# Kernel tuning notes

Measured on AMD Instinct MI355X. Metric: run time of the kernel, lower is better.

Reference implementation:

```python
import jax, jax.numpy as jnp
import numpy as np

N = 50000        # nodes
E = 1600000      # edges (avg degree 32)
H = 128          # hidden_channels == num_filters
G = 50           # num_gaussians
L = 5            # num_interactions
CUTOFF = 4.5
VOCAB = 100
LOG2 = float(np.log(2.0))


def setup_inputs() -> dict:
    key = jax.random.key(0)
    ks = jax.random.split(key, 12)
    s = 1.0 / np.sqrt(H)
    sg = 1.0 / np.sqrt(G)
    atomic_numbers = jax.random.randint(ks[0], (N,), 0, VOCAB, dtype=jnp.int32)
    edge_index = jax.random.randint(ks[1], (2, E), 0, N, dtype=jnp.int32)
    edge_attr = jax.random.uniform(ks[2], (E,), dtype=jnp.float32)
    emb = jax.random.normal(ks[3], (VOCAB, H), dtype=jnp.float32) * 0.1
    emb = emb.at[0].set(0.0)  # padding_idx=0
    Wi = jax.random.normal(ks[4], (L, H, H), dtype=jnp.float32) * s
    bi = jnp.zeros((L, H), dtype=jnp.float32)
    Wn = jax.random.normal(ks[5], (L, G, H), dtype=jnp.float32) * sg
    bn = jnp.zeros((L, H), dtype=jnp.float32)
    Wo = jax.random.normal(ks[6], (L, H, H), dtype=jnp.float32) * s
    bo = jnp.zeros((L, H), dtype=jnp.float32)
    Wl = jax.random.normal(ks[7], (L, H, H), dtype=jnp.float32) * s
    bl = jnp.zeros((L, H), dtype=jnp.float32)
    return {"atomic_numbers": atomic_numbers, "edge_index": edge_index,
            "edge_attr": edge_attr, "emb": emb,
            "Wi": Wi, "bi": bi, "Wn": Wn, "bn": bn,
            "Wo": Wo, "bo": bo, "Wl": Wl, "bl": bl}


def _gaussian_smearing(dist):
    offsets = jnp.linspace(0.0, CUTOFF, G, dtype=jnp.float32)
    coeff = -0.5 / (offsets[1] - offsets[0]) ** 2
    return jnp.exp(coeff * (dist[:, None] - offsets[None, :]) ** 2)  # [E, G]


def reference(atomic_numbers, edge_index, edge_attr, emb,
              Wi, bi, Wn, bn, Wo, bo, Wl, bl):
    src, dst = edge_index[0], edge_index[1]
    x = emb[atomic_numbers]                      # [N, H]
    gauss = _gaussian_smearing(edge_attr)        # [E, G]
    C = 0.5 * (jnp.cos(edge_attr * jnp.pi / CUTOFF) + 1.0)  # cosine cutoff [E]
    for l in range(L):
        W = (gauss @ Wn[l] + bn[l]) * C[:, None]   # edge filters [E, H]
        h = x @ Wi[l] + bi[l]                       # [N, H]
        msg = h[src] * W                            # gather + filter [E, H]
        agg = jax.ops.segment_sum(msg, dst, num_segments=N)  # scatter-add [N, H]
        h = agg @ Wo[l] + bo[l]
        h = jax.nn.softplus(h) - LOG2               # shifted softplus
        h = h @ Wl[l] + bl[l]
        x = x + h                                   # residual
    return x
```

## Files before the change

### kernel.cpp

```cpp
#include <hip/hip_runtime.h>
#include <hip/hip_bf16.h>

#define HDIM 128
#define NG 50
#define NL 5
#define TBN 4096
#define CAP 96
#define CAPB 9000
#define CHUNK 8192

static constexpr float CUTOFF_F = 4.5f;
static constexpr float PI_F = 3.14159265358979323846f;
static constexpr float LN2_F = 0.6931471805599453f;

typedef __attribute__((ext_vector_type(8))) short bf16x8;
typedef __attribute__((ext_vector_type(4))) float f32x4;

__device__ __forceinline__ unsigned f2bfbits(float f) {
    unsigned b = __float_as_uint(f);
    return (b + 0x7FFFu + ((b >> 16) & 1u)) >> 16;
}
__device__ __forceinline__ float bflo(unsigned u) { return __uint_as_float(u << 16); }
__device__ __forceinline__ float bfhi(unsigned u) { return __uint_as_float(u & 0xFFFF0000u); }

__device__ __forceinline__ float softplus_shifted(float v) {
    return fmaxf(v, 0.0f) + log1pf(__expf(-fabsf(v))) - LN2_F;
}

__device__ __forceinline__ bf16x8 ldB(const unsigned short* __restrict__ W,
                                      int nn, int kc, int l4) {
    return *reinterpret_cast<const bf16x8*>(W + nn * HDIM + kc * 32 + l4 * 8);
}

__global__ __launch_bounds__(256) void embed_kernel(
    const int* __restrict__ an, const float* __restrict__ emb,
    float* __restrict__ x, int n)
{
    int idx = blockIdx.x * 256 + threadIdx.x;
    int total = n * (HDIM / 4);
    if (idx >= total) return;
    int i = idx >> 5;
    int j = idx & 31;
    int a = an[i];
    reinterpret_cast<float4*>(x)[(size_t)i * 32 + j] =
        reinterpret_cast<const float4*>(emb)[(size_t)a * 32 + j];
}

__global__ __launch_bounds__(256) void prep_weights(
    const float* __restrict__ Wi, const float* __restrict__ Wo,
    const float* __restrict__ Wl, unsigned short* __restrict__ Wt)
{
    int b = blockIdx.x;
    int l = b / 3, m = b % 3;
    const float* src = (m == 0 ? Wi : (m == 1 ? Wo : Wl)) + (size_t)l * HDIM * HDIM;
    unsigned short* dst = Wt + (size_t)b * HDIM * HDIM;
    for (int idx = threadIdx.x; idx < HDIM * HDIM; idx += 256) {
        int k = idx >> 7, n = idx & 127;
        dst[n * HDIM + k] = (unsigned short)f2bfbits(src[k * HDIM + n]);
    }
}

__global__ __launch_bounds__(128) void build_tables_all(
    const float* __restrict__ Wn, const float* __restrict__ bn,
    unsigned short* __restrict__ T)
{
    __shared__ float gs[NG];
    int p = blockIdx.x;
    int l = blockIdx.y;
    int j = threadIdx.x;
    const float* Wnl = Wn + (size_t)l * NG * HDIM;
    float d = (float)p * (1.0f / (float)TBN);
    if (j < NG) {
        const float delta = CUTOFF_F / (float)(NG - 1);
        const float coeff = -0.5f / (delta * delta);
        float t = d - (float)j * delta;
        gs[j] = expf(coeff * t * t);
    }
    __syncthreads();
    float acc = bn[(size_t)l * HDIM + j];
    #pragma unroll 10
    for (int g = 0; g < NG; ++g) acc = fmaf(gs[g], Wnl[g * HDIM + j], acc);
    acc *= 0.5f * (cosf(d * (PI_F / CUTOFF_F)) + 1.0f);
    T[((size_t)l * (TBN + 1) + p) * HDIM + j] = (unsigned short)f2bfbits(acc);
}

__global__ __launch_bounds__(512) void bucket_pass(
    const int* __restrict__ src, const int* __restrict__ dstp,
    const float* __restrict__ attr, int* __restrict__ gbase,
    uint2* __restrict__ buf, int E, int nbuck)
{
    __shared__ int hist[256], cur[256], base_l[256];
    const int tid = threadIdx.x;
    if (tid < 256) { hist[tid] = 0; cur[tid] = 0; }
    __syncthreads();
    const int e0 = blockIdx.x * CHUNK;
    const int e1 = min(e0 + CHUNK, E);
    for (int e = e0 + tid; e < e1; e += 512)
        atomicAdd(&hist[dstp[e] >> 8], 1);
    __syncthreads();
    if (tid < nbuck)
        base_l[tid] = hist[tid] ? atomicAdd(&gbase[tid], hist[tid]) : 0;
    __syncthreads();
    for (int e = e0 + tid; e < e1; e += 512) {
        int d = dstp[e];
        int b = d >> 8;
        int rank = atomicAdd(&cur[b], 1);
        int pos = base_l[b] + rank;
        unsigned ii = (unsigned)(int)fminf(attr[e] * (float)TBN + 0.5f, (float)TBN);
        if (pos < CAPB)
            buf[(size_t)b * CAPB + pos] = make_uint2((ii << 16) | (unsigned)src[e], (unsigned)d);
    }
}

__global__ __launch_bounds__(512) void bin_pass(
    const int* __restrict__ gtot, const uint2* __restrict__ buf,
    unsigned* __restrict__ sp, int* __restrict__ cnt, int N)
{
    __shared__ int cl[256];
    const int b = blockIdx.x;
    const int tid = threadIdx.x;
    if (tid < 256) cl[tid] = 0;
    __syncthreads();
    int total = gtot[b];
    if (total > CAPB) total = CAPB;
    const uint2* rb = buf + (size_t)b * CAPB;
    for (int i = tid; i < total; i += 512) {
        uint2 r = rb[i];
        int node = (int)r.y;
        int slot = atomicAdd(&cl[node & 255], 1);
        if (slot < CAP) sp[(size_t)node * CAP + slot] = r.x;
    }
    __syncthreads();
    if (tid < 256) {
        int node = b * 256 + tid;
        if (node < N) cnt[node] = min(cl[tid], CAP);
    }
}

__global__ __launch_bounds__(256) void mfma_gemm0(
    const float* __restrict__ A, const unsigned short* __restrict__ Wt,
    const float* __restrict__ bias, unsigned short* __restrict__ outp, int M)
{
    __shared__ unsigned short Al[64 * HDIM];
    __shared__ unsigned short Hs[64 * HDIM];
    const int tid = threadIdx.x;
    const int row0 = blockIdx.x * 64;

    #pragma unroll
    for (int it = 0; it < 8; ++it) {
        int idx = it * 256 + tid;
        int r = idx >> 5;
        int k2 = (idx & 31) * 8;
        int row = row0 + r;
        float4 v = make_float4(0.f, 0.f, 0.f, 0.f);
        if (row < M) v = reinterpret_cast<const float4*>(A)[(size_t)row * 32 + (idx & 31)];
        uint2 u;
        u.x = f2bfbits(v.x) | (f2bfbits(v.y) << 16);
        u.y = f2bfbits(v.z) | (f2bfbits(v.w) << 16);
        *reinterpret_cast<uint2*>(reinterpret_cast<char*>(Al) +
            r * 256 + (k2 ^ ((r & 7) << 4))) = u;
    }
    __syncthreads();

    const int wid = tid >> 6, lane = tid & 63;
    const int wr = wid >> 1, wc = wid & 1;
    const int l15 = lane & 15, l4 = lane >> 4;

    f32x4 acc[2][4] = {};
    bf16x8 afrag[2][4];
    #pragma unroll
    for (int m = 0; m < 2; ++m)
        #pragma unroll
        for (int kc = 0; kc < 4; ++kc) {
            int r = wr * 32 + m * 16 + l15;
            int k2 = (kc * 32 + l4 * 8) * 2;
            afrag[m][kc] = *reinterpret_cast<const bf16x8*>(
                reinterpret_cast<const char*>(Al) + r * 256 + (k2 ^ ((r & 7) << 4)));
        }
    #pragma unroll
    for (int n = 0; n < 4; ++n)
        #pragma unroll
        for (int kc = 0; kc < 4; ++kc) {
            bf16x8 bfrag = ldB(Wt, wc * 64 + n * 16 + l15, kc, l4);
            #pragma unroll
            for (int m = 0; m < 2; ++m)
                acc[m][n] = __builtin_amdgcn_mfma_f32_16x16x32_bf16(
                    afrag[m][kc], bfrag, acc[m][n], 0, 0, 0);
        }
    #pragma unroll
    for (int n = 0; n < 4; ++n) {
        int col = wc * 64 + n * 16 + l15;
        float bv = bias[col];
        #pragma unroll
        for (int m = 0; m < 2; ++m)
            #pragma unroll
            for (int r = 0; r < 4; ++r) {
                int rl = wr * 32 + m * 16 + l4 * 4 + r;
                Hs[rl * HDIM + col] = (unsigned short)f2bfbits(acc[m][n][r] + bv);
            }
    }
    __syncthreads();
    #pragma unroll
    for (int it = 0; it < 4; ++it) {
        int e = it * 256 + tid;
        int row = row0 + (e >> 4);
        if (row < M)
            reinterpret_cast<uint4*>(outp)[(size_t)row0 * 16 + e] =
                reinterpret_cast<const uint4*>(Hs)[e];
    }
}

template<int LAST>
__global__ __launch_bounds__(256) void gemm_fused(
    const unsigned short* __restrict__ aggb, const unsigned short* __restrict__ Wot,
    const float* __restrict__ bo, const unsigned short* __restrict__ Wlt,
    const float* __restrict__ bl, float* __restrict__ x,
    const unsigned short* __restrict__ Wit, const float* __restrict__ bi_,
    unsigned short* __restrict__ hb, int M)
{
    __shared__ unsigned short Al[64 * HDIM];
    __shared__ unsigned short Hs[64 * HDIM];
    const int tid = threadIdx.x;
    const int row0 = blockIdx.x * 64;

    #pragma unroll
    for (int it = 0; it < 4; ++it) {
        int idx = it * 256 + tid;
        int r = idx >> 4;
        int k2 = (idx & 15) * 16;
        int row = row0 + r;
        uint4 v = make_uint4(0, 0, 0, 0);
        if (row < M) v = reinterpret_cast<const uint4*>(aggb)[(size_t)row * 16 + (idx & 15)];
        *reinterpret_cast<uint4*>(reinterpret_cast<char*>(Al) +
            r * 256 + (k2 ^ ((r & 7) << 4))) = v;
    }
    __syncthreads();

    const int wid = tid >> 6, lane = tid & 63;
    const int wr = wid >> 1, wc = wid & 1;
    const int l15 = lane & 15, l4 = lane >> 4;

    f32x4 acc1[2][4] = {};
    bf16x8 afrag[2][4];
    #pragma unroll
    for (int m = 0; m < 2; ++m)
        #pragma unroll
        for (int kc = 0; kc < 4; ++kc) {
            int r = wr * 32 + m * 16 + l15;
            int k2 = (kc * 32 + l4 * 8) * 2;
            afrag[m][kc] = *reinterpret_cast<const bf16x8*>(
                reinterpret_cast<const char*>(Al) + r * 256 + (k2 ^ ((r & 7) << 4)));
        }
    #pragma unroll
    for (int n = 0; n < 4; ++n)
        #pragma unroll
        for (int kc = 0; kc < 4; ++kc) {
            bf16x8 bfrag = ldB(Wot, wc * 64 + n * 16 + l15, kc, l4);
            #pragma unroll
            for (int m = 0; m < 2; ++m)
                acc1[m][n] = __builtin_amdgcn_mfma_f32_16x16x32_bf16(
                    afrag[m][kc], bfrag, acc1[m][n], 0, 0, 0);
        }
    __syncthreads();

    #pragma unroll
    for (int n = 0; n < 4; ++n) {
        int col = wc * 64 + n * 16 + l15;
        float bv = bo[col];
        #pragma unroll
        for (int m = 0; m < 2; ++m)
            #pragma unroll
            for (int r = 0; r < 4; ++r) {
                int rl = wr * 32 + m * 16 + l4 * 4 + r;
                float v = softplus_shifted(acc1[m][n][r] + bv);
                *reinterpret_cast<unsigned short*>(reinterpret_cast<char*>(Al) +
                    rl * 256 + ((2 * col) ^ ((rl & 7) << 4))) = (unsigned short)f2bfbits(v);
            }
    }
    __syncthreads();

    f32x4 acc2[2][4] = {};
    #pragma unroll
    for (int m = 0; m < 2; ++m)
        #pragma unroll
        for (int kc = 0; kc < 4; ++kc) {
            int r = wr * 32 + m * 16 + l15;
            int k2 = (kc * 32 + l4 * 8) * 2;
            afrag[m][kc] = *reinterpret_cast<const bf16x8*>(
                reinterpret_cast<const char*>(Al) + r * 256 + (k2 ^ ((r & 7) << 4)));
        }
    #pragma unroll
    for (int n = 0; n < 4; ++n)
        #pragma unroll
        for (int kc = 0; kc < 4; ++kc) {
            bf16x8 bfrag = ldB(Wlt, wc * 64 + n * 16 + l15, kc, l4);
            #pragma unroll
            for (int m = 0; m < 2; ++m)
                acc2[m][n] = __builtin_amdgcn_mfma_f32_16x16x32_bf16(
                    afrag[m][kc], bfrag, acc2[m][n], 0, 0, 0);
        }
    __syncthreads();

    #pragma unroll
    for (int n = 0; n < 4; ++n) {
        int col = wc * 64 + n * 16 + l15;
        float bv = bl[col];
        #pragma unroll
        for (int m = 0; m < 2; ++m)
            #pragma unroll
            for (int r = 0; r < 4; ++r) {
                int rl = wr * 32 + m * 16 + l4 * 4 + r;
                int row = row0 + rl;
                float v = acc2[m][n][r] + bv;
                if (row < M) {
                    float* o = x + (size_t)row * HDIM + col;
                    v += *o;
                    *o = v;
                }
                if (!LAST)
                    *reinterpret_cast<unsigned short*>(reinterpret_cast<char*>(Al) +
                        rl * 256 + ((2 * col) ^ ((rl & 7) << 4))) = (unsigned short)f2bfbits(v);
            }
    }
    if (LAST) return;
    __syncthreads();

    f32x4 acc3[2][4] = {};
    #pragma unroll
    for (int m = 0; m < 2; ++m)
        #pragma unroll
        for (int kc = 0; kc < 4; ++kc) {
            int r = wr * 32 + m * 16 + l15;
            int k2 = (kc * 32 + l4 * 8) * 2;
            afrag[m][kc] = *reinterpret_cast<const bf16x8*>(
                reinterpret_cast<const char*>(Al) + r * 256 + (k2 ^ ((r & 7) << 4)));
        }
    #pragma unroll
    for (int n = 0; n < 4; ++n)
        #pragma unroll
        for (int kc = 0; kc < 4; ++kc) {
            bf16x8 bfrag = ldB(Wit, wc * 64 + n * 16 + l15, kc, l4);
            #pragma unroll
            for (int m = 0; m < 2; ++m)
                acc3[m][n] = __builtin_amdgcn_mfma_f32_16x16x32_bf16(
                    afrag[m][kc], bfrag, acc3[m][n], 0, 0, 0);
        }
    #pragma unroll
    for (int n = 0; n < 4; ++n) {
        int col = wc * 64 + n * 16 + l15;
        float bv = bi_[col];
        #pragma unroll
        for (int m = 0; m < 2; ++m)
            #pragma unroll
            for (int r = 0; r < 4; ++r) {
                int rl = wr * 32 + m * 16 + l4 * 4 + r;
                Hs[rl * HDIM + col] = (unsigned short)f2bfbits(acc3[m][n][r] + bv);
            }
    }
    __syncthreads();
    #pragma unroll
    for (int it = 0; it < 4; ++it) {
        int e = it * 256 + tid;
        int row = row0 + (e >> 4);
        if (row < M)
            reinterpret_cast<uint4*>(hb)[(size_t)row0 * 16 + e] =
                reinterpret_cast<const uint4*>(Hs)[e];
    }
}

__global__ __launch_bounds__(256) void agg_kernel(
    const int* __restrict__ cnt, const unsigned* __restrict__ sp,
    const unsigned short* __restrict__ T,
    const unsigned* __restrict__ hb,
    unsigned* __restrict__ aggb, int n)
{
    __shared__ float2 part[2][64];
    const int tid = threadIdx.x;
    const int lane = tid & 63;
    const int wv = tid >> 6;
    const int pair = wv >> 1, half = wv & 1;
    const int node = blockIdx.x * 2 + pair;

    int deg = (node < n) ? cnt[node] : 0;
    const unsigned* recs = sp + (size_t)node * CAP;
    int d2 = deg >> 1;
    int i  = half ? d2 : 0;
    int i1 = half ? deg : d2;
    float ax = 0.0f, ay = 0.0f;

    for (; i + 8 <= i1; i += 8) {
        unsigned rec[8], tv[8], hv[8];
        #pragma unroll
        for (int k = 0; k < 8; ++k) rec[k] = recs[i + k];
        #pragma unroll
        for (int k = 0; k < 8; ++k) {
            tv[k] = reinterpret_cast<const unsigned*>(T + (size_t)(rec[k] >> 16) * HDIM)[lane];
            hv[k] = hb[(size_t)(rec[k] & 0xFFFFu) * 64 + lane];
        }
        #pragma unroll
        for (int k = 0; k < 8; ++k) {
            ax = fmaf(bflo(hv[k]), bflo(tv[k]), ax);
            ay = fmaf(bfhi(hv[k]), bfhi(tv[k]), ay);
        }
    }
    if (i + 4 <= i1) {
        unsigned rec[4], tv[4], hv[4];
        #pragma unroll
        for (int k = 0; k < 4; ++k) rec[k] = recs[i + k];
        #pragma unroll
        for (int k = 0; k < 4; ++k) {
            tv[k] = reinterpret_cast<const unsigned*>(T + (size_t)(rec[k] >> 16) * HDIM)[lane];
            hv[k] = hb[(size_t)(rec[k] & 0xFFFFu) * 64 + lane];
        }
        #pragma unroll
        for (int k = 0; k < 4; ++k) {
            ax = fmaf(bflo(hv[k]), bflo(tv[k]), ax);
            ay = fmaf(bfhi(hv[k]), bfhi(tv[k]), ay);
        }
        i += 4;
    }
    for (; i < i1; ++i) {
        unsigned rec = recs[i];
        unsigned tvv = reinterpret_cast<const unsigned*>(T + (size_t)(rec >> 16) * HDIM)[lane];
        unsigned hvv = hb[(size_t)(rec & 0xFFFFu) * 64 + lane];
        ax = fmaf(bflo(hvv), bflo(tvv), ax);
        ay = fmaf(bfhi(hvv), bfhi(tvv), ay);
    }

    if (half) part[pair][lane] = make_float2(ax, ay);
    __syncthreads();
    if (!half && node < n) {
        float2 p = part[pair][lane];
        ax += p.x; ay += p.y;
        aggb[(size_t)node * 64 + lane] = f2bfbits(ax) | (f2bfbits(ay) << 16);
    }
}

extern "C" void kernel_launch(void* const* d_in, const int* in_sizes, int n_in,
                              void* d_out, int out_size, void* d_ws, size_t ws_size,
                              hipStream_t stream)
{
    const int*   an   = (const int*)d_in[0];
    const int*   ei   = (const int*)d_in[1];
    const float* attr = (const float*)d_in[2];
    const float* emb  = (const float*)d_in[3];
    const float* Wi   = (const float*)d_in[4];
    const float* bi   = (const float*)d_in[5];
    const float* Wn   = (const float*)d_in[6];
    const float* bn   = (const float*)d_in[7];
    const float* Wo   = (const float*)d_in[8];
    const float* bo   = (const float*)d_in[9];
    const float* Wl   = (const float*)d_in[10];
    const float* bl   = (const float*)d_in[11];

    const int N = in_sizes[0];
    const int E = in_sizes[2];
    const int* srcp = ei;
    const int* dstp = ei + E;
    const int nbuck = (N + 255) >> 8;

    float* x = (float*)d_out;

    char* w = (char*)d_ws;
    unsigned*       aggb = (unsigned*)w;      w += (size_t)N * HDIM * 2;
    unsigned*       hb   = (unsigned*)w;      w += (size_t)N * HDIM * 2;
    unsigned short* T    = (unsigned short*)w; w += (size_t)NL * (TBN + 1) * HDIM * 2;
    unsigned short* Wt   = (unsigned short*)w; w += (size_t)NL * 3 * HDIM * HDIM * 2;
    int*            cnt  = (int*)w;           w += (size_t)N * 4;
    int*            gbase= (int*)w;           w += 256 * 4;
    unsigned*       sp   = (unsigned*)w;      w += (size_t)N * CAP * 4;
    uint2*          buf  = (uint2*)aggb;

    prep_weights<<<NL * 3, 256, 0, stream>>>(Wi, Wo, Wl, Wt);
    embed_kernel<<<(N * 32 + 255) / 256, 256, 0, stream>>>(an, emb, x, N);
    build_tables_all<<<dim3(TBN + 1, NL), 128, 0, stream>>>(Wn, bn, T);

    hipMemsetAsync(gbase, 0, 256 * sizeof(int), stream);
    bucket_pass<<<(E + CHUNK - 1) / CHUNK, 512, 0, stream>>>(
        srcp, dstp, attr, gbase, buf, E, nbuck);
    bin_pass<<<nbuck, 512, 0, stream>>>(gbase, buf, sp, cnt, N);

    const int gemm_grid = (N + 63) / 64;
    const int agg_grid  = (N + 1) / 2;

    mfma_gemm0<<<gemm_grid, 256, 0, stream>>>(x, Wt, bi, (unsigned short*)hb, N);

    for (int l = 0; l < NL; ++l) {
        agg_kernel<<<agg_grid, 256, 0, stream>>>(
            cnt, sp, T + (size_t)l * (TBN + 1) * HDIM, hb, aggb, N);
        if (l < NL - 1) {
            gemm_fused<0><<<gemm_grid, 256, 0, stream>>>(
                (unsigned short*)aggb, Wt + (size_t)(l * 3 + 1) * HDIM * HDIM, bo + (size_t)l * HDIM,
                Wt + (size_t)(l * 3 + 2) * HDIM * HDIM, bl + (size_t)l * HDIM, x,
                Wt + (size_t)((l + 1) * 3 + 0) * HDIM * HDIM, bi + (size_t)(l + 1) * HDIM,
                (unsigned short*)hb, N);
        } else {
            gemm_fused<1><<<gemm_grid, 256, 0, stream>>>(
                (unsigned short*)aggb, Wt + (size_t)(l * 3 + 1) * HDIM * HDIM, bo + (size_t)l * HDIM,
                Wt + (size_t)(l * 3 + 2) * HDIM * HDIM, bl + (size_t)l * HDIM, x,
                Wt, bi, (unsigned short*)hb, N);
        }
    }
}
```

Before: 806.3 us.

## Use 512-thread single LDS buffer in fused GEMM and load A fragments directly

The fused three-GEMM kernel now runs 8 waves per 64-row block, each wave owning a 16x64 tile instead of 32x64. A fragments are read straight from global memory rather than staged through LDS. The two shared buffers are merged into one, with extra barriers so a buffer is never overwritten while still being read. Softplus switches to the fast __logf. The goal is less LDS and fewer registers per wave for higher occupancy, at the cost of more barriers, uncoalesced direct fragment loads, and each wave refetching the B weights for half the work.

```diff
diff --git a/kernel.cpp b/kernel.cpp
--- a/kernel.cpp
+++ b/kernel.cpp
@@ -24,7 +24,7 @@
 __device__ __forceinline__ float bfhi(unsigned u) { return __uint_as_float(u & 0xFFFF0000u); }
 
 __device__ __forceinline__ float softplus_shifted(float v) {
-    return fmaxf(v, 0.0f) + log1pf(__expf(-fabsf(v))) - LN2_F;
+    return fmaxf(v, 0.0f) + __logf(1.0f + __expf(-fabsf(v))) - LN2_F;
 }
 
 __device__ __forceinline__ bf16x8 ldB(const unsigned short* __restrict__ W,
@@ -141,8 +141,7 @@
     const float* __restrict__ A, const unsigned short* __restrict__ Wt,
     const float* __restrict__ bias, unsigned short* __restrict__ outp, int M)
 {
-    __shared__ unsigned short Al[64 * HDIM];
-    __shared__ unsigned short Hs[64 * HDIM];
+    __shared__ unsigned short Ls[64 * HDIM];
     const int tid = threadIdx.x;
     const int row0 = blockIdx.x * 64;
 
@@ -157,7 +156,7 @@
         uint2 u;
         u.x = f2bfbits(v.x) | (f2bfbits(v.y) << 16);
         u.y = f2bfbits(v.z) | (f2bfbits(v.w) << 16);
-        *reinterpret_cast<uint2*>(reinterpret_cast<char*>(Al) +
+        *reinterpret_cast<uint2*>(reinterpret_cast<char*>(Ls) +
             r * 256 + (k2 ^ ((r & 7) << 4))) = u;
     }
     __syncthreads();
@@ -175,8 +174,9 @@
             int r = wr * 32 + m * 16 + l15;
             int k2 = (kc * 32 + l4 * 8) * 2;
             afrag[m][kc] = *reinterpret_cast<const bf16x8*>(
-                reinterpret_cast<const char*>(Al) + r * 256 + (k2 ^ ((r & 7) << 4)));
-        }
+                reinterpret_cast<const char*>(Ls) + r * 256 + (k2 ^ ((r & 7) << 4)));
+        }
+    __syncthreads();
     #pragma unroll
     for (int n = 0; n < 4; ++n)
         #pragma unroll
@@ -196,7 +196,7 @@
             #pragma unroll
             for (int r = 0; r < 4; ++r) {
                 int rl = wr * 32 + m * 16 + l4 * 4 + r;
-                Hs[rl * HDIM + col] = (unsigned short)f2bfbits(acc[m][n][r] + bv);
+                Ls[rl * HDIM + col] = (unsigned short)f2bfbits(acc[m][n][r] + bv);
             }
     }
     __syncthreads();
@@ -206,165 +206,131 @@
         int row = row0 + (e >> 4);
         if (row < M)
             reinterpret_cast<uint4*>(outp)[(size_t)row0 * 16 + e] =
-                reinterpret_cast<const uint4*>(Hs)[e];
+                reinterpret_cast<const uint4*>(Ls)[e];
     }
 }
 
 template<int LAST>
-__global__ __launch_bounds__(256) void gemm_fused(
+__global__ __launch_bounds__(512) void gemm_fused(
     const unsigned short* __restrict__ aggb, const unsigned short* __restrict__ Wot,
     const float* __restrict__ bo, const unsigned short* __restrict__ Wlt,
     const float* __restrict__ bl, float* __restrict__ x,
     const unsigned short* __restrict__ Wit, const float* __restrict__ bi_,
     unsigned short* __restrict__ hb, int M)
 {
-    __shared__ unsigned short Al[64 * HDIM];
-    __shared__ unsigned short Hs[64 * HDIM];
+    __shared__ unsigned short Ls[64 * HDIM];
     const int tid = threadIdx.x;
     const int row0 = blockIdx.x * 64;
-
-    #pragma unroll
-    for (int it = 0; it < 4; ++it) {
-        int idx = it * 256 + tid;
-        int r = idx >> 4;
-        int k2 = (idx & 15) * 16;
-        int row = row0 + r;
-        uint4 v = make_uint4(0, 0, 0, 0);
-        if (row < M) v = reinterpret_cast<const uint4*>(aggb)[(size_t)row * 16 + (idx & 15)];
-        *reinterpret_cast<uint4*>(reinterpret_cast<char*>(Al) +
-            r * 256 + (k2 ^ ((r & 7) << 4))) = v;
-    }
-    __syncthreads();
-
     const int wid = tid >> 6, lane = tid & 63;
     const int wr = wid >> 1, wc = wid & 1;
     const int l15 = lane & 15, l4 = lane >> 4;
 
-    f32x4 acc1[2][4] = {};
-    bf16x8 afrag[2][4];
-    #pragma unroll
-    for (int m = 0; m < 2; ++m)
-        #pragma unroll
-        for (int kc = 0; kc < 4; ++kc) {
-            int r = wr * 32 + m * 16 + l15;
-            int k2 = (kc * 32 + l4 * 8) * 2;
-            afrag[m][kc] = *reinterpret_cast<const bf16x8*>(
-                reinterpret_cast<const char*>(Al) + r * 256 + (k2 ^ ((r & 7) << 4)));
-        }
+    const unsigned short* ag =
+        aggb + (size_t)(row0 + wr * 16 + l15) * HDIM + l4 * 8;
+    f32x4 acc1[4] = {};
+    bf16x8 af[4];
+    #pragma unroll
+    for (int kc = 0; kc < 4; ++kc)
+        af[kc] = *reinterpret_cast<const bf16x8*>(ag + kc * 32);
     #pragma unroll
     for (int n = 0; n < 4; ++n)
         #pragma unroll
         for (int kc = 0; kc < 4; ++kc) {
             bf16x8 bfrag = ldB(Wot, wc * 64 + n * 16 + l15, kc, l4);
-            #pragma unroll
-            for (int m = 0; m < 2; ++m)
-                acc1[m][n] = __builtin_amdgcn_mfma_f32_16x16x32_bf16(
-                    afrag[m][kc], bfrag, acc1[m][n], 0, 0, 0);
-        }
-    __syncthreads();
+            acc1[n] = __builtin_amdgcn_mfma_f32_16x16x32_bf16(af[kc], bfrag, acc1[n], 0, 0, 0);
+        }
 
     #pragma unroll
     for (int n = 0; n < 4; ++n) {
         int col = wc * 64 + n * 16 + l15;
         float bv = bo[col];
         #pragma unroll
-        for (int m = 0; m < 2; ++m)
-            #pragma unroll
-            for (int r = 0; r < 4; ++r) {
-                int rl = wr * 32 + m * 16 + l4 * 4 + r;
-                float v = softplus_shifted(acc1[m][n][r] + bv);
-                *reinterpret_cast<unsigned short*>(reinterpret_cast<char*>(Al) +
-                    rl * 256 + ((2 * col) ^ ((rl & 7) << 4))) = (unsigned short)f2bfbits(v);
-            }
-    }
-    __syncthreads();
-
-    f32x4 acc2[2][4] = {};
-    #pragma unroll
-    for (int m = 0; m < 2; ++m)
-        #pragma unroll
-        for (int kc = 0; kc < 4; ++kc) {
-            int r = wr * 32 + m * 16 + l15;
+        for (int r = 0; r < 4; ++r) {
+            int rl = wr * 16 + l4 * 4 + r;
+            float v = softplus_shifted(acc1[n][r] + bv);
+            *reinterpret_cast<unsigned short*>(reinterpret_cast<char*>(Ls) +
+                rl * 256 + ((2 * col) ^ ((rl & 7) << 4))) = (unsigned short)f2bfbits(v);
+        }
+    }
+    __syncthreads();
+
+    {
+        int r = wr * 16 + l15;
+        #pragma unroll
+        for (int kc = 0; kc < 4; ++kc) {
             int k2 = (kc * 32 + l4 * 8) * 2;
-            afrag[m][kc] = *reinterpret_cast<const bf16x8*>(
-                reinterpret_cast<const char*>(Al) + r * 256 + (k2 ^ ((r & 7) << 4)));
-        }
+            af[kc] = *reinterpret_cast<const bf16x8*>(
+                reinterpret_cast<const char*>(Ls) + r * 256 + (k2 ^ ((r & 7) << 4)));
+        }
+    }
+    __syncthreads();
+    f32x4 acc2[4] = {};
     #pragma unroll
     for (int n = 0; n < 4; ++n)
         #pragma unroll
         for (int kc = 0; kc < 4; ++kc) {
             bf16x8 bfrag = ldB(Wlt, wc * 64 + n * 16 + l15, kc, l4);
-            #pragma unroll
-            for (int m = 0; m < 2; ++m)
-                acc2[m][n] = __builtin_amdgcn_mfma_f32_16x16x32_bf16(
-                    afrag[m][kc], bfrag, acc2[m][n], 0, 0, 0);
-        }
-    __syncthreads();
+            acc2[n] = __builtin_amdgcn_mfma_f32_16x16x32_bf16(af[kc], bfrag, acc2[n], 0, 0, 0);
+        }
 
     #pragma unroll
     for (int n = 0; n < 4; ++n) {
         int col = wc * 64 + n * 16 + l15;
         float bv = bl[col];
         #pragma unroll
-        for (int m = 0; m < 2; ++m)
-            #pragma unroll
-            for (int r = 0; r < 4; ++r) {
-                int rl = wr * 32 + m * 16 + l4 * 4 + r;
-                int row = row0 + rl;
-                float v = acc2[m][n][r] + bv;
-                if (row < M) {
-                    float* o = x + (size_t)row * HDIM + col;
-                    v += *o;
-                    *o = v;
-                }
-                if (!LAST)
-                    *reinterpret_cast<unsigned short*>(reinterpret_cast<char*>(Al) +
-                        rl * 256 + ((2 * col) ^ ((rl & 7) << 4))) = (unsigned short)f2bfbits(v);
+        for (int r = 0; r < 4; ++r) {
+            int rl = wr * 16 + l4 * 4 + r;
+            int row = row0 + rl;
+            float v = acc2[n][r] + bv;
+            if (row < M) {
+                float* o = x + (size_t)row * HDIM + col;
+                v += *o;
+                *o = v;
             }
+            if (!LAST)
+                *reinterpret_cast<unsigned short*>(reinterpret_cast<char*>(Ls) +
+                    rl * 256 + ((2 * col) ^ ((rl & 7) << 4))) = (unsigned short)f2bfbits(v);
+        }
     }
     if (LAST) return;
     __syncthreads();
 
-    f32x4 acc3[2][4] = {};
-    #pragma unroll
-    for (int m = 0; m < 2; ++m)
-        #pragma unroll
-        for (int kc = 0; kc < 4; ++kc) {
-            int r = wr * 32 + m * 16 + l15;
+    {
+        int r = wr * 16 + l15;
+        #pragma unroll
+        for (int kc = 0; kc < 4; ++kc) {
             int k2 = (kc * 32 + l4 * 8) * 2;
-            afrag[m][kc] = *reinterpret_cast<const bf16x8*>(
-                reinterpret_cast<const char*>(Al) + r * 256 + (k2 ^ ((r & 7) << 4)));
-        }
+            af[kc] = *reinterpret_cast<const bf16x8*>(
+                reinterpret_cast<const char*>(Ls) + r * 256 + (k2 ^ ((r & 7) << 4)));
+        }
+    }
+    __syncthreads();
+    f32x4 acc3[4] = {};
     #pragma unroll
     for (int n = 0; n < 4; ++n)
         #pragma unroll
         for (int kc = 0; kc < 4; ++kc) {
             bf16x8 bfrag = ldB(Wit, wc * 64 + n * 16 + l15, kc, l4);
-            #pragma unroll
-            for (int m = 0; m < 2; ++m)
-                acc3[m][n] = __builtin_amdgcn_mfma_f32_16x16x32_bf16(
-                    afrag[m][kc], bfrag, acc3[m][n], 0, 0, 0);
+            acc3[n] = __builtin_amdgcn_mfma_f32_16x16x32_bf16(af[kc], bfrag, acc3[n], 0, 0, 0);
         }
     #pragma unroll
     for (int n = 0; n < 4; ++n) {
         int col = wc * 64 + n * 16 + l15;
         float bv = bi_[col];
         #pragma unroll
-        for (int m = 0; m < 2; ++m)
-            #pragma unroll
-            for (int r = 0; r < 4; ++r) {
-                int rl = wr * 32 + m * 16 + l4 * 4 + r;
-                Hs[rl * HDIM + col] = (unsigned short)f2bfbits(acc3[m][n][r] + bv);
-            }
-    }
-    __syncthreads();
-    #pragma unroll
-    for (int it = 0; it < 4; ++it) {
-        int e = it * 256 + tid;
+        for (int r = 0; r < 4; ++r) {
+            int rl = wr * 16 + l4 * 4 + r;
+            Ls[rl * HDIM + col] = (unsigned short)f2bfbits(acc3[n][r] + bv);
+        }
+    }
+    __syncthreads();
+    #pragma unroll
+    for (int it = 0; it < 2; ++it) {
+        int e = it * 512 + tid;
         int row = row0 + (e >> 4);
         if (row < M)
             reinterpret_cast<uint4*>(hb)[(size_t)row0 * 16 + e] =
-                reinterpret_cast<const uint4*>(Hs)[e];
+                reinterpret_cast<const uint4*>(Ls)[e];
     }
 }
 
@@ -489,13 +455,13 @@
         agg_kernel<<<agg_grid, 256, 0, stream>>>(
             cnt, sp, T + (size_t)l * (TBN + 1) * HDIM, hb, aggb, N);
         if (l < NL - 1) {
-            gemm_fused<0><<<gemm_grid, 256, 0, stream>>>(
+            gemm_fused<0><<<gemm_grid, 512, 0, stream>>>(
                 (unsigned short*)aggb, Wt + (size_t)(l * 3 + 1) * HDIM * HDIM, bo + (size_t)l * HDIM,
                 Wt + (size_t)(l * 3 + 2) * HDIM * HDIM, bl + (size_t)l * HDIM, x,
                 Wt + (size_t)((l + 1) * 3 + 0) * HDIM * HDIM, bi + (size_t)(l + 1) * HDIM,
                 (unsigned short*)hb, N);
         } else {
-            gemm_fused<1><<<gemm_grid, 256, 0, stream>>>(
+            gemm_fused<1><<<gemm_grid, 512, 0, stream>>>(
                 (unsigned short*)aggb, Wt + (size_t)(l * 3 + 1) * HDIM * HDIM, bo + (size_t)l * HDIM,
                 Wt + (size_t)(l * 3 + 2) * HDIM * HDIM, bl + (size_t)l * HDIM, x,
                 Wt, bi, (unsigned short*)hb, N);
```

New measurement: 835.5 us. 3.6% more time.
